# Kernel optimization log

Measured on AMD Instinct MI355X. Metric: run time of the kernel, lower is better.

Reference implementation:

```python
import jax, jax.numpy as jnp
import numpy as np

N, E, D, R = 50000, 1200000, 128, 6  # nodes, edges, channels (dim_in==dim_out), relations
NEG_SLOPE = 0.2


def setup_inputs() -> dict:
    key = jax.random.key(0)
    ks = jax.random.split(key, 7)
    x = jax.random.normal(ks[0], (N, D), jnp.float32)
    edge_index = jax.random.randint(ks[1], (2, E), 0, N)
    edge_type = jax.random.randint(ks[2], (E,), 0, R)
    # RGATConv params (heads=1): weight [R, D, D], q/k [D, 1], bias [D]
    weight = jax.random.normal(ks[3], (R, D, D), jnp.float32) * 0.05
    q = jax.random.normal(ks[4], (D, 1), jnp.float32) * 0.05
    k = jax.random.normal(ks[5], (D, 1), jnp.float32) * 0.05
    bias = jnp.zeros((D,), jnp.float32)
    return dict(x=x, edge_index=edge_index, edge_type=edge_type,
                weight=weight, q=q, k=k, bias=bias)


def segment_softmax(logits, seg, num_segments):
    m = jax.ops.segment_max(logits, seg, num_segments=num_segments)
    m = jnp.where(jnp.isfinite(m), m, 0.0)  # empty segments -> 0
    e = jnp.exp(logits - m[seg])
    s = jax.ops.segment_sum(e, seg, num_segments=num_segments)
    return e / (s[seg] + 1e-16)


def reference(x, edge_index, edge_type, weight, q, k, bias):
    src, dst = edge_index[0], edge_index[1]  # message flows src(j) -> dst(i)
    # per-node, per-relation transform W_r x_n : [R, N, D]
    hx = jnp.einsum('nd,rdo->rno', x, weight)
    # attention projections (heads=1): scalar per node per relation
    nq = jnp.einsum('rno,o->rn', hx, q[:, 0])  # q_i component
    nk = jnp.einsum('rno,o->rn', hx, k[:, 0])  # k_j component
    # additive self-attention, across-relation softmax over incoming edges
    logits = jax.nn.leaky_relu(nq[edge_type, dst] + nk[edge_type, src], NEG_SLOPE)
    alpha = segment_softmax(logits, dst, N)  # [E]
    # message = alpha * (W_r x_j), scatter-add into dst; dropout inactive (eval)
    msg = alpha[:, None] * hx[edge_type, src]  # [E, D]
    agg = jax.ops.segment_sum(msg, dst, num_segments=N) + bias
    out = agg + x  # residual add in GATLayer.forward
    return out, alpha[:, None]  # attention weights: [E, heads=1]
```

## Files before the change

### kernel.cpp

```cpp
#include <hip/hip_runtime.h>
#include <hip/hip_bf16.h>
#include <cstdint>

#define NN 50000
#define NE 1200000
#define DD 128
#define RR 6
#define NEG 0.2f
#define NB 391
#define CAP 4096
#define TILE 4096
#define GEMMB 782
#define SCB ((NE + TILE - 1) / TILE)

typedef __hip_bfloat16 bf16;
typedef __attribute__((ext_vector_type(8))) short short8;
typedef __attribute__((ext_vector_type(4))) float f32x4;

__device__ __forceinline__ float bflo(unsigned u) { return __uint_as_float(u << 16); }
__device__ __forceinline__ float bfhi(unsigned u) { return __uint_as_float(u & 0xFFFF0000u); }
__device__ __forceinline__ ushort f2b(float v) {
  unsigned b = __float_as_uint(v);
  return (ushort)((b + 0x7FFFu + ((b >> 16) & 1u)) >> 16);
}

__global__ __launch_bounds__(256) void k_prep(const float* __restrict__ W,
    const float* __restrict__ qv, const float* __restrict__ kv,
    ushort* __restrict__ wp, ushort* __restrict__ wp7, int* __restrict__ bcur) {
  int t = blockIdx.x * 256 + threadIdx.x;
  if (t < NB) bcur[t] = 0;
  if (t < RR * 8 * 4 * 64) {
    int lane = t & 63;
    int ks = (t >> 6) & 3;
    int cf = (t >> 8) & 7;
    int r = t >> 11;
    int col = cf * 16 + (lane & 15);
    int k0 = ks * 32 + (lane >> 4) * 8;
    ushort* dst = wp + (size_t)t * 8;
    #pragma unroll
    for (int e = 0; e < 8; ++e)
      dst[e] = f2b(W[((size_t)r * DD + (k0 + e)) * DD + col]);
  } else if (t < RR * 8 * 4 * 64 + 256) {
    int idx = t - RR * 8 * 4 * 64;
    int lane = idx & 63, ks = idx >> 6;
    int col = lane & 15;
    int k0 = ks * 32 + (lane >> 4) * 8;
    ushort* dst = wp7 + (size_t)idx * 8;
    #pragma unroll
    for (int e = 0; e < 8; ++e) {
      float v = 0.f;
      if (col < 12) {
        int r = col < 6 ? col : col - 6;
        const float* vv = col < 6 ? qv : kv;
        const float* row = W + ((size_t)r * DD + (k0 + e)) * DD;
        for (int o = 0; o < DD; ++o) v += row[o] * vv[o];
      }
      dst[e] = f2b(v);
    }
  }
}

union FSMem {
  ushort tile[64][136];
  struct {
    unsigned sval[TILE];
    unsigned short sbkt[TILE];
    int lh[NB], lbase[NB], lcur[NB];
  } c;
};

__global__ __launch_bounds__(256) void k_fused(const float* __restrict__ x,
    const ushort* __restrict__ wp, const ushort* __restrict__ wp7,
    const int* __restrict__ ei, const int* __restrict__ et,
    int* __restrict__ bcur, unsigned* __restrict__ bedge,
    ushort* __restrict__ hx, float* __restrict__ nq, float* __restrict__ nk) {
  __shared__ FSMem sm;
  int tid = threadIdx.x;

  if (blockIdx.x >= GEMMB) {
    int blk = blockIdx.x - GEMMB;
    int e0 = blk * TILE;
    int lim = NE - e0; if (lim > TILE) lim = TILE;
    for (int i = tid; i < NB; i += 256) sm.c.lh[i] = 0;
    __syncthreads();
    for (int i = tid; i < lim; i += 256) {
      int e = e0 + i;
      int s = ei[e], d = ei[NE + e], r = et[e];
      unsigned rowid = (unsigned)(r * NN + s);
      sm.c.sval[i] = (rowid << 3) | (unsigned)r | ((unsigned)(d & 127) << 22);
      sm.c.sbkt[i] = (unsigned short)(d >> 7);
      atomicAdd(&sm.c.lh[d >> 7], 1);
    }
    __syncthreads();
    for (int i = tid; i < NB; i += 256) {
      int c = sm.c.lh[i];
      sm.c.lbase[i] = c ? atomicAdd(&bcur[i], c) : 0;
      sm.c.lcur[i] = 0;
    }
    __syncthreads();
    for (int i = tid; i < lim; i += 256) {
      int b = sm.c.sbkt[i];
      int pos = b * CAP + sm.c.lbase[b] + atomicAdd(&sm.c.lcur[b], 1);
      bedge[pos] = sm.c.sval[i];
    }
    return;
  }

  int w = tid >> 6, l = tid & 63;
  int wrow = w & 1, wcol = w >> 1;
  int row0 = blockIdx.x * 64;
  int rbase = row0 + wrow * 32;
  int lr = l & 15, lg = l >> 4;

  short8 af[2][4];
  #pragma unroll
  for (int rf = 0; rf < 2; ++rf) {
    int row = rbase + rf * 16 + lr;
    row = row < NN ? row : NN - 1;
    const float* src = x + (size_t)row * DD + lg * 8;
    #pragma unroll
    for (int ks = 0; ks < 4; ++ks) {
      float4 u0 = *reinterpret_cast<const float4*>(src + ks * 32);
      float4 u1 = *reinterpret_cast<const float4*>(src + ks * 32 + 4);
      short8 a;
      a[0] = (short)f2b(u0.x); a[1] = (short)f2b(u0.y);
      a[2] = (short)f2b(u0.z); a[3] = (short)f2b(u0.w);
      a[4] = (short)f2b(u1.x); a[5] = (short)f2b(u1.y);
      a[6] = (short)f2b(u1.z); a[7] = (short)f2b(u1.w);
      af[rf][ks] = a;
    }
  }

  if (wcol == 0) {
    f32x4 aq0 = {0.f, 0.f, 0.f, 0.f}, aq1 = {0.f, 0.f, 0.f, 0.f};
    #pragma unroll
    for (int ks = 0; ks < 4; ++ks) {
      short8 b = *reinterpret_cast<const short8*>(wp7 + (size_t)(ks * 64 + l) * 8);
      aq0 = __builtin_amdgcn_mfma_f32_16x16x32_bf16(af[0][ks], b, aq0, 0, 0, 0);
      aq1 = __builtin_amdgcn_mfma_f32_16x16x32_bf16(af[1][ks], b, aq1, 0, 0, 0);
    }
    if (lr < 12) {
      float* pl = (lr < 6 ? nq + (size_t)lr * NN : nk + (size_t)(lr - 6) * NN);
      #pragma unroll
      for (int rf = 0; rf < 2; ++rf) {
        int rowb = rbase + rf * 16 + lg * 4;
        f32x4 v = rf ? aq1 : aq0;
        if (rowb + 3 < NN) {
          float4 o4 = make_float4(v[0], v[1], v[2], v[3]);
          *reinterpret_cast<float4*>(pl + rowb) = o4;
        } else {
          #pragma unroll
          for (int j = 0; j < 4; ++j) if (rowb + j < NN) pl[rowb + j] = v[j];
        }
      }
    }
  }

  for (int r = 0; r < RR; ++r) {
    #pragma unroll
    for (int cfl = 0; cfl < 4; ++cfl) {
      int cfg = wcol * 4 + cfl;
      const ushort* bp = wp + (((size_t)(r * 8 + cfg) * 4) * 64 + l) * 8;
      short8 b0 = *reinterpret_cast<const short8*>(bp);
      short8 b1 = *reinterpret_cast<const short8*>(bp + 512);
      short8 b2 = *reinterpret_cast<const short8*>(bp + 1024);
      short8 b3 = *reinterpret_cast<const short8*>(bp + 1536);
      f32x4 acc0 = {0.f, 0.f, 0.f, 0.f};
      f32x4 acc1 = {0.f, 0.f, 0.f, 0.f};
      acc0 = __builtin_amdgcn_mfma_f32_16x16x32_bf16(af[0][0], b0, acc0, 0, 0, 0);
      acc1 = __builtin_amdgcn_mfma_f32_16x16x32_bf16(af[1][0], b0, acc1, 0, 0, 0);
      acc0 = __builtin_amdgcn_mfma_f32_16x16x32_bf16(af[0][1], b1, acc0, 0, 0, 0);
      acc1 = __builtin_amdgcn_mfma_f32_16x16x32_bf16(af[1][1], b1, acc1, 0, 0, 0);
      acc0 = __builtin_amdgcn_mfma_f32_16x16x32_bf16(af[0][2], b2, acc0, 0, 0, 0);
      acc1 = __builtin_amdgcn_mfma_f32_16x16x32_bf16(af[1][2], b2, acc1, 0, 0, 0);
      acc0 = __builtin_amdgcn_mfma_f32_16x16x32_bf16(af[0][3], b3, acc0, 0, 0, 0);
      acc1 = __builtin_amdgcn_mfma_f32_16x16x32_bf16(af[1][3], b3, acc1, 0, 0, 0);

      int col = cfg * 16 + lr;
      #pragma unroll
      for (int rf = 0; rf < 2; ++rf) {
        int rowrel = wrow * 32 + rf * 16 + lg * 4;
        f32x4 ac = rf ? acc1 : acc0;
        #pragma unroll
        for (int j = 0; j < 4; ++j)
          sm.tile[rowrel + j][col] = f2b(ac[j]);
      }
    }
    __syncthreads();
    #pragma unroll
    for (int it = 0; it < 4; ++it) {
      int rowrel = (tid >> 4) + it * 16;
      int grow = row0 + rowrel;
      uint4 v = *reinterpret_cast<const uint4*>(&sm.tile[rowrel][(tid & 15) * 8]);
      if (grow < NN)
        *reinterpret_cast<uint4*>(hx + ((size_t)r * NN + grow) * DD + (tid & 15) * 8) = v;
    }
    __syncthreads();
  }
}

__global__ __launch_bounds__(1024) void k_bfinal(const unsigned* __restrict__ bedge,
    const int* __restrict__ bcur,
    const float* __restrict__ nq, const float* __restrict__ nk,
    int* __restrict__ deg, int* __restrict__ offs, unsigned* __restrict__ rec) {
  __shared__ int lh[128], sc_s[128], lcur[128];
  int b = blockIdx.x, tid = threadIdx.x;
  int base = b * CAP, cnt = bcur[b];
  if (tid < 128) lh[tid] = 0;
  __syncthreads();
  for (int i = tid; i < cnt; i += 1024)
    atomicAdd(&lh[(bedge[base + i] >> 22) & 127], 1);
  __syncthreads();
  int v = 0;
  if (tid < 128) { v = lh[tid]; sc_s[tid] = v; }
  __syncthreads();
  for (int off = 1; off < 128; off <<= 1) {
    int u = (tid < 128 && tid >= off) ? sc_s[tid - off] : 0;
    __syncthreads();
    if (tid < 128) sc_s[tid] += u;
    __syncthreads();
  }
  if (tid < 128) {
    int excl = sc_s[tid] - v;
    int n = (b << 7) + tid;
    if (n < NN) { deg[n] = v; offs[n] = base + excl; }
    lcur[tid] = base + excl;
  }
  __syncthreads();
  for (int i = tid; i < cnt; i += 1024) {
    unsigned be = bedge[base + i];
    unsigned rowid = (be >> 3) & 0x7FFFFu;
    int r = (int)(be & 7u);
    int dloc = (int)((be >> 22) & 127u);
    float l = nq[(size_t)r * NN + (b << 7) + dloc] + nk[rowid];
    l = l > 0.f ? l : NEG * l;
    float p = __expf(l);
    unsigned pb = (__float_as_uint(p) + 0x20000u) >> 18;
    int pos = atomicAdd(&lcur[dloc], 1);
    rec[pos] = (rowid << 13) | (pb & 0x1FFFu);
  }
}

__global__ __launch_bounds__(256) void k_agg(const float* __restrict__ x,
    const float* __restrict__ bias, const int* __restrict__ offs,
    const int* __restrict__ deg, const unsigned* __restrict__ rec,
    const bf16* __restrict__ hx, float* __restrict__ out,
    float* __restrict__ irec) {
  int g = threadIdx.x >> 5, lane = threadIdx.x & 31;
  int n = blockIdx.x * 8 + g;
  if (n >= NN) return;
  int base = offs[n], cnt = deg[n];
  const char* hp = (const char*)hx;
  int lo8 = lane * 8;

  float ssum = 0.f;
  float a0 = 0.f, a1 = 0.f, a2 = 0.f, a3 = 0.f;

#define DEC(E, OFF, P) unsigned OFF = ((E) >> 5) & 0xFFFFFF00u; \
                       float P = __uint_as_float(((E) & 0x1FFFu) << 18);

  int j = 0;
  for (; j + 7 < cnt; j += 8) {
    unsigned e0 = rec[base + j],     e1 = rec[base + j + 1];
    unsigned e2 = rec[base + j + 2], e3 = rec[base + j + 3];
    unsigned e4 = rec[base + j + 4], e5 = rec[base + j + 5];
    unsigned e6 = rec[base + j + 6], e7 = rec[base + j + 7];
    DEC(e0, o0, p0) DEC(e1, o1, p1) DEC(e2, o2, p2) DEC(e3, o3, p3)
    DEC(e4, o4, p4) DEC(e5, o5, p5) DEC(e6, o6, p6) DEC(e7, o7, p7)
    uint2 q0 = *reinterpret_cast<const uint2*>(hp + o0 + lo8);
    uint2 q1 = *reinterpret_cast<const uint2*>(hp + o1 + lo8);
    uint2 q2 = *reinterpret_cast<const uint2*>(hp + o2 + lo8);
    uint2 q3 = *reinterpret_cast<const uint2*>(hp + o3 + lo8);
    uint2 q4 = *reinterpret_cast<const uint2*>(hp + o4 + lo8);
    uint2 q5 = *reinterpret_cast<const uint2*>(hp + o5 + lo8);
    uint2 q6 = *reinterpret_cast<const uint2*>(hp + o6 + lo8);
    uint2 q7 = *reinterpret_cast<const uint2*>(hp + o7 + lo8);
    ssum += ((p0 + p1) + (p2 + p3)) + ((p4 + p5) + (p6 + p7));
    a0 += p0 * bflo(q0.x) + p1 * bflo(q1.x) + p2 * bflo(q2.x) + p3 * bflo(q3.x)
        + p4 * bflo(q4.x) + p5 * bflo(q5.x) + p6 * bflo(q6.x) + p7 * bflo(q7.x);
    a1 += p0 * bfhi(q0.x) + p1 * bfhi(q1.x) + p2 * bfhi(q2.x) + p3 * bfhi(q3.x)
        + p4 * bfhi(q4.x) + p5 * bfhi(q5.x) + p6 * bfhi(q6.x) + p7 * bfhi(q7.x);
    a2 += p0 * bflo(q0.y) + p1 * bflo(q1.y) + p2 * bflo(q2.y) + p3 * bflo(q3.y)
        + p4 * bflo(q4.y) + p5 * bflo(q5.y) + p6 * bflo(q6.y) + p7 * bflo(q7.y);
    a3 += p0 * bfhi(q0.y) + p1 * bfhi(q1.y) + p2 * bfhi(q2.y) + p3 * bfhi(q3.y)
        + p4 * bfhi(q4.y) + p5 * bfhi(q5.y) + p6 * bfhi(q6.y) + p7 * bfhi(q7.y);
  }
  for (; j + 3 < cnt; j += 4) {
    unsigned e0 = rec[base + j],     e1 = rec[base + j + 1];
    unsigned e2 = rec[base + j + 2], e3 = rec[base + j + 3];
    DEC(e0, o0, p0) DEC(e1, o1, p1) DEC(e2, o2, p2) DEC(e3, o3, p3)
    uint2 q0 = *reinterpret_cast<const uint2*>(hp + o0 + lo8);
    uint2 q1 = *reinterpret_cast<const uint2*>(hp + o1 + lo8);
    uint2 q2 = *reinterpret_cast<const uint2*>(hp + o2 + lo8);
    uint2 q3 = *reinterpret_cast<const uint2*>(hp + o3 + lo8);
    ssum += (p0 + p1) + (p2 + p3);
    a0 += p0 * bflo(q0.x) + p1 * bflo(q1.x) + p2 * bflo(q2.x) + p3 * bflo(q3.x);
    a1 += p0 * bfhi(q0.x) + p1 * bfhi(q1.x) + p2 * bfhi(q2.x) + p3 * bfhi(q3.x);
    a2 += p0 * bflo(q0.y) + p1 * bflo(q1.y) + p2 * bflo(q2.y) + p3 * bflo(q3.y);
    a3 += p0 * bfhi(q0.y) + p1 * bfhi(q1.y) + p2 * bfhi(q2.y) + p3 * bfhi(q3.y);
  }
  for (; j < cnt; ++j) {
    unsigned e0 = rec[base + j];
    DEC(e0, o0, p0)
    uint2 q0 = *reinterpret_cast<const uint2*>(hp + o0 + lo8);
    ssum += p0;
    a0 += p0 * bflo(q0.x);
    a1 += p0 * bfhi(q0.x);
    a2 += p0 * bflo(q0.y);
    a3 += p0 * bfhi(q0.y);
  }
#undef DEC

  float inv = 1.f / (ssum + 1e-16f);
  size_t o = (size_t)n * DD + lane * 4;
  float4 xb = *reinterpret_cast<const float4*>(x + o);
  float4 bb = *reinterpret_cast<const float4*>(bias + lane * 4);
  float4 res;
  res.x = xb.x + bb.x + a0 * inv;
  res.y = xb.y + bb.y + a1 * inv;
  res.z = xb.z + bb.z + a2 * inv;
  res.w = xb.w + bb.w + a3 * inv;
  *reinterpret_cast<float4*>(out + o) = res;

  if (lane == 0) irec[n] = inv;
}

__global__ __launch_bounds__(256) void k_alpha(const int* __restrict__ ei,
    const int* __restrict__ et, const float* __restrict__ nq,
    const float* __restrict__ nk, const float* __restrict__ irec,
    float* __restrict__ alpha) {
  int e = (blockIdx.x * 256 + threadIdx.x) * 2;
  if (e >= NE) return;
  int2 ss = *reinterpret_cast<const int2*>(ei + e);
  int2 dd = *reinterpret_cast<const int2*>(ei + NE + e);
  int2 rr = *reinterpret_cast<const int2*>(et + e);
  float l0 = nq[(size_t)rr.x * NN + dd.x] + nk[(size_t)rr.x * NN + ss.x];
  float l1 = nq[(size_t)rr.y * NN + dd.y] + nk[(size_t)rr.y * NN + ss.y];
  l0 = l0 > 0.f ? l0 : NEG * l0;
  l1 = l1 > 0.f ? l1 : NEG * l1;
  float2 res;
  res.x = __expf(l0) * irec[dd.x];
  res.y = __expf(l1) * irec[dd.y];
  *reinterpret_cast<float2*>(alpha + e) = res;
}

extern "C" void kernel_launch(void* const* d_in, const int* in_sizes, int n_in,
                              void* d_out, int out_size, void* d_ws, size_t ws_size,
                              hipStream_t stream) {
  const float* x    = (const float*)d_in[0];
  const int*   ei   = (const int*)d_in[1];
  const int*   et   = (const int*)d_in[2];
  const float* W    = (const float*)d_in[3];
  const float* qv   = (const float*)d_in[4];
  const float* kv   = (const float*)d_in[5];
  const float* bias = (const float*)d_in[6];

  float* out   = (float*)d_out;
  float* alpha = out + (size_t)NN * DD;

  char* p = (char*)d_ws;
  bf16*  hx      = (bf16*)p;    p += (size_t)RR * NN * DD * sizeof(bf16);
  float* nq      = (float*)p;   p += (size_t)RR * NN * sizeof(float);
  float* nk      = (float*)p;   p += (size_t)RR * NN * sizeof(float);
  int*   deg     = (int*)p;     p += NN * sizeof(int);
  int*   offs    = (int*)p;     p += NN * sizeof(int);
  float* irec    = (float*)p;   p += NN * sizeof(float);
  int*   bcur    = (int*)p;     p += NB * sizeof(int);
  p = (char*)(((uintptr_t)p + 15) & ~(uintptr_t)15);
  unsigned* bedge = (unsigned*)p; p += (size_t)NB * CAP * sizeof(unsigned);
  unsigned* rec  = (unsigned*)p;  p += (size_t)NB * CAP * sizeof(unsigned);
  ushort* wp     = (ushort*)p;  p += (size_t)RR * 8 * 4 * 64 * 8 * sizeof(ushort);
  ushort* wp7    = (ushort*)p;  p += (size_t)4 * 64 * 8 * sizeof(ushort);

  k_prep<<<49, 256, 0, stream>>>(W, qv, kv, wp, wp7, bcur);
  k_fused<<<GEMMB + SCB, 256, 0, stream>>>(x, wp, wp7, ei, et, bcur, bedge,
                                           (ushort*)hx, nq, nk);
  k_bfinal<<<NB, 1024, 0, stream>>>(bedge, bcur, nq, nk, deg, offs, rec);
  k_agg<<<(NN + 7) / 8, 256, 0, stream>>>(x, bias, offs, deg, rec, hx, out, irec);
  k_alpha<<<(NE / 2 + 255) / 256, 256, 0, stream>>>(ei, et, nq, nk, irec, alpha);
}
```

Before: 159.2 us.

## Compute softmax denominators in bucket finalize and merge aggregation with alpha kernel

The per-node softmax denominator is now accumulated with shared-memory atomics in k_bfinal, using the same quantized exponent values that are stored in the edge records, and written to irec there. Because alpha no longer waits on the aggregation kernel, the aggregation and alpha kernels become one launch whose blocks are interleaved between the two roles, removing a kernel boundary and letting gather-heavy and streaming work overlap. In exchange, k_bfinal does extra shared float atomics per edge, and alpha blocks share the launch with the heavier aggregation blocks.

```diff
diff --git a/kernel.cpp b/kernel.cpp
--- a/kernel.cpp
+++ b/kernel.cpp
@@ -12,6 +12,9 @@
 #define TILE 4096
 #define GEMMB 782
 #define SCB ((NE + TILE - 1) / TILE)
+#define AGGB ((NN + 7) / 8)
+#define ALPB ((NE / 2 + 255) / 256)
+#define TAILB (AGGB + ALPB)
 
 typedef __hip_bfloat16 bf16;
 typedef __attribute__((ext_vector_type(8))) short short8;
@@ -202,11 +205,13 @@
 __global__ __launch_bounds__(1024) void k_bfinal(const unsigned* __restrict__ bedge,
     const int* __restrict__ bcur,
     const float* __restrict__ nq, const float* __restrict__ nk,
-    int* __restrict__ deg, int* __restrict__ offs, unsigned* __restrict__ rec) {
+    int* __restrict__ deg, int* __restrict__ offs, unsigned* __restrict__ rec,
+    float* __restrict__ irec) {
   __shared__ int lh[128], sc_s[128], lcur[128];
+  __shared__ float ssb[128];
   int b = blockIdx.x, tid = threadIdx.x;
   int base = b * CAP, cnt = bcur[b];
-  if (tid < 128) lh[tid] = 0;
+  if (tid < 128) { lh[tid] = 0; ssb[tid] = 0.f; }
   __syncthreads();
   for (int i = tid; i < cnt; i += 1024)
     atomicAdd(&lh[(bedge[base + i] >> 22) & 127], 1);
@@ -235,25 +240,55 @@
     float l = nq[(size_t)r * NN + (b << 7) + dloc] + nk[rowid];
     l = l > 0.f ? l : NEG * l;
     float p = __expf(l);
-    unsigned pb = (__float_as_uint(p) + 0x20000u) >> 18;
+    unsigned pb = ((__float_as_uint(p) + 0x20000u) >> 18) & 0x1FFFu;
+    atomicAdd(&ssb[dloc], __uint_as_float(pb << 18));
     int pos = atomicAdd(&lcur[dloc], 1);
-    rec[pos] = (rowid << 13) | (pb & 0x1FFFu);
-  }
-}
-
-__global__ __launch_bounds__(256) void k_agg(const float* __restrict__ x,
+    rec[pos] = (rowid << 13) | pb;
+  }
+  __syncthreads();
+  if (tid < 128) {
+    int n = (b << 7) + tid;
+    if (n < NN) irec[n] = 1.f / (ssb[tid] + 1e-16f);
+  }
+}
+
+__global__ __launch_bounds__(256) void k_tail(const float* __restrict__ x,
     const float* __restrict__ bias, const int* __restrict__ offs,
     const int* __restrict__ deg, const unsigned* __restrict__ rec,
-    const bf16* __restrict__ hx, float* __restrict__ out,
-    float* __restrict__ irec) {
+    const bf16* __restrict__ hx, const int* __restrict__ ei,
+    const int* __restrict__ et, const float* __restrict__ nq,
+    const float* __restrict__ nk, const float* __restrict__ irec,
+    float* __restrict__ out, float* __restrict__ alpha) {
+  int bid = blockIdx.x;
+  int ab0 = (int)(((long long)bid * ALPB) / TAILB);
+  int ab1 = (int)(((long long)(bid + 1) * ALPB) / TAILB);
+
+  if (ab1 > ab0) {
+    int e = (ab0 * 256 + threadIdx.x) * 2;
+    if (e >= NE) return;
+    int2 ss = *reinterpret_cast<const int2*>(ei + e);
+    int2 dd = *reinterpret_cast<const int2*>(ei + NE + e);
+    int2 rr = *reinterpret_cast<const int2*>(et + e);
+    float l0 = nq[(size_t)rr.x * NN + dd.x] + nk[(size_t)rr.x * NN + ss.x];
+    float l1 = nq[(size_t)rr.y * NN + dd.y] + nk[(size_t)rr.y * NN + ss.y];
+    l0 = l0 > 0.f ? l0 : NEG * l0;
+    l1 = l1 > 0.f ? l1 : NEG * l1;
+    float2 res;
+    res.x = __expf(l0) * irec[dd.x];
+    res.y = __expf(l1) * irec[dd.y];
+    *reinterpret_cast<float2*>(alpha + e) = res;
+    return;
+  }
+
+  int gb = bid - ab0;
   int g = threadIdx.x >> 5, lane = threadIdx.x & 31;
-  int n = blockIdx.x * 8 + g;
+  int n = gb * 8 + g;
   if (n >= NN) return;
   int base = offs[n], cnt = deg[n];
   const char* hp = (const char*)hx;
   int lo8 = lane * 8;
-
-  float ssum = 0.f;
+  float inv = irec[n];
+
   float a0 = 0.f, a1 = 0.f, a2 = 0.f, a3 = 0.f;
 
 #define DEC(E, OFF, P) unsigned OFF = ((E) >> 5) & 0xFFFFFF00u; \
@@ -275,7 +310,6 @@
     uint2 q5 = *reinterpret_cast<const uint2*>(hp + o5 + lo8);
     uint2 q6 = *reinterpret_cast<const uint2*>(hp + o6 + lo8);
     uint2 q7 = *reinterpret_cast<const uint2*>(hp + o7 + lo8);
-    ssum += ((p0 + p1) + (p2 + p3)) + ((p4 + p5) + (p6 + p7));
     a0 += p0 * bflo(q0.x) + p1 * bflo(q1.x) + p2 * bflo(q2.x) + p3 * bflo(q3.x)
         + p4 * bflo(q4.x) + p5 * bflo(q5.x) + p6 * bflo(q6.x) + p7 * bflo(q7.x);
     a1 += p0 * bfhi(q0.x) + p1 * bfhi(q1.x) + p2 * bfhi(q2.x) + p3 * bfhi(q3.x)
@@ -293,7 +327,6 @@
     uint2 q1 = *reinterpret_cast<const uint2*>(hp + o1 + lo8);
     uint2 q2 = *reinterpret_cast<const uint2*>(hp + o2 + lo8);
     uint2 q3 = *reinterpret_cast<const uint2*>(hp + o3 + lo8);
-    ssum += (p0 + p1) + (p2 + p3);
     a0 += p0 * bflo(q0.x) + p1 * bflo(q1.x) + p2 * bflo(q2.x) + p3 * bflo(q3.x);
     a1 += p0 * bfhi(q0.x) + p1 * bfhi(q1.x) + p2 * bfhi(q2.x) + p3 * bfhi(q3.x);
     a2 += p0 * bflo(q0.y) + p1 * bflo(q1.y) + p2 * bflo(q2.y) + p3 * bflo(q3.y);
@@ -303,7 +336,6 @@
     unsigned e0 = rec[base + j];
     DEC(e0, o0, p0)
     uint2 q0 = *reinterpret_cast<const uint2*>(hp + o0 + lo8);
-    ssum += p0;
     a0 += p0 * bflo(q0.x);
     a1 += p0 * bfhi(q0.x);
     a2 += p0 * bflo(q0.y);
@@ -311,7 +343,6 @@
   }
 #undef DEC
 
-  float inv = 1.f / (ssum + 1e-16f);
   size_t o = (size_t)n * DD + lane * 4;
   float4 xb = *reinterpret_cast<const float4*>(x + o);
   float4 bb = *reinterpret_cast<const float4*>(bias + lane * 4);
@@ -321,27 +352,6 @@
   res.z = xb.z + bb.z + a2 * inv;
   res.w = xb.w + bb.w + a3 * inv;
   *reinterpret_cast<float4*>(out + o) = res;
-
-  if (lane == 0) irec[n] = inv;
-}
-
-__global__ __launch_bounds__(256) void k_alpha(const int* __restrict__ ei,
-    const int* __restrict__ et, const float* __restrict__ nq,
-    const float* __restrict__ nk, const float* __restrict__ irec,
-    float* __restrict__ alpha) {
-  int e = (blockIdx.x * 256 + threadIdx.x) * 2;
-  if (e >= NE) return;
-  int2 ss = *reinterpret_cast<const int2*>(ei + e);
-  int2 dd = *reinterpret_cast<const int2*>(ei + NE + e);
-  int2 rr = *reinterpret_cast<const int2*>(et + e);
-  float l0 = nq[(size_t)rr.x * NN + dd.x] + nk[(size_t)rr.x * NN + ss.x];
-  float l1 = nq[(size_t)rr.y * NN + dd.y] + nk[(size_t)rr.y * NN + ss.y];
-  l0 = l0 > 0.f ? l0 : NEG * l0;
-  l1 = l1 > 0.f ? l1 : NEG * l1;
-  float2 res;
-  res.x = __expf(l0) * irec[dd.x];
-  res.y = __expf(l1) * irec[dd.y];
-  *reinterpret_cast<float2*>(alpha + e) = res;
 }
 
 extern "C" void kernel_launch(void* const* d_in, const int* in_sizes, int n_in,
@@ -375,7 +385,7 @@
   k_prep<<<49, 256, 0, stream>>>(W, qv, kv, wp, wp7, bcur);
   k_fused<<<GEMMB + SCB, 256, 0, stream>>>(x, wp, wp7, ei, et, bcur, bedge,
                                            (ushort*)hx, nq, nk);
-  k_bfinal<<<NB, 1024, 0, stream>>>(bedge, bcur, nq, nk, deg, offs, rec);
-  k_agg<<<(NN + 7) / 8, 256, 0, stream>>>(x, bias, offs, deg, rec, hx, out, irec);
-  k_alpha<<<(NE / 2 + 255) / 256, 256, 0, stream>>>(ei, et, nq, nk, irec, alpha);
-}
+  k_bfinal<<<NB, 1024, 0, stream>>>(bedge, bcur, nq, nk, deg, offs, rec, irec);
+  k_tail<<<TAILB, 256, 0, stream>>>(x, bias, offs, deg, rec, hx, ei, et,
+                                    nq, nk, irec, out, alpha);
+}
```

New measurement: 163.7 us. +2.8%, slower.
